# Kernel tuning notes

Measured on AMD Instinct MI355X. Metric: run time of the kernel, lower is better.

Reference implementation:

```python
import jax, jax.numpy as jnp
import numpy as np

B, SEQ, D = 4, 1024, 1024
H = 16
HD = D // H            # 64, matches cos/sin last dim
S_COLS, TOPK = 8, 2
INTER = 768            # find_multiple(round(1.0 * D * 2 / 3), 256)
EPS = 1e-5


def setup_inputs() -> dict:
    key = jax.random.key(0)
    ks = jax.random.split(key, 6)
    hidden_states = jax.random.normal(ks[0], (B, SEQ, D), jnp.float32)
    # RoPE tables (standard rotary, theta=10000)
    inv_freq = 1.0 / (10000.0 ** (jnp.arange(0, HD, 2, dtype=jnp.float32) / HD))
    freqs = jnp.outer(jnp.arange(SEQ, dtype=jnp.float32), inv_freq)
    emb = jnp.concatenate([freqs, freqs], axis=-1)  # [SEQ, HD]
    cos, sin = jnp.cos(emb), jnp.sin(emb)
    Wr = jax.random.normal(ks[1], (S_COLS, D), jnp.float32) * 0.02
    temperature = jnp.ones((1,), jnp.float32)
    # Stacked per-column TransformerBlock params (bias-free linears)
    Wqkv = jax.random.normal(ks[2], (S_COLS, D, 3 * D), jnp.float32) * 0.02
    Wo = jax.random.normal(ks[3], (S_COLS, D, D), jnp.float32) * 0.02
    Wgu = jax.random.normal(ks[4], (S_COLS, D, 2 * INTER), jnp.float32) * 0.02
    Wd = jax.random.normal(ks[5], (S_COLS, INTER, D), jnp.float32) * 0.02
    return dict(hidden_states=hidden_states, cos=cos, sin=sin, Wr=Wr,
                temperature=temperature, Wqkv=Wqkv, Wo=Wo, Wgu=Wgu, Wd=Wd)


def _rms_norm(x):
    return x * jax.lax.rsqrt(jnp.mean(x * x, axis=-1, keepdims=True) + EPS)


def _rotate_half(x):
    x1, x2 = jnp.split(x, 2, axis=-1)
    return jnp.concatenate([-x2, x1], axis=-1)


def _columns_forward(x, Wqkv, Wo, Wgu, Wd, cos, sin):
    # x: [n, seq, D] dispatched sequences; params gathered per dispatch entry [n, ...]
    n, seq, d = x.shape
    qkv = jnp.einsum('nsd,nde->nse', x, Wqkv)
    q, k, v = jnp.split(qkv, 3, axis=-1)
    q = q.reshape(n, seq, H, HD)
    k = k.reshape(n, seq, H, HD)
    v = v.reshape(n, seq, H, HD)
    c = cos[None, :, None, :]
    s = sin[None, :, None, :]
    q = q * c + _rotate_half(q) * s
    k = k * c + _rotate_half(k) * s
    scores = jnp.einsum('nqhd,nkhd->nhqk', q, k) / jnp.sqrt(jnp.asarray(HD, x.dtype))
    attn = jax.nn.softmax(scores, axis=-1)  # non-causal (HRM-style block)
    ctx = jnp.einsum('nhqk,nkhd->nqhd', attn, v).reshape(n, seq, d)
    attn_out = jnp.einsum('nsd,nde->nse', ctx, Wo)
    x = _rms_norm(x + attn_out)                      # post-norm residual
    gu = jnp.einsum('nsd,nde->nse', x, Wgu)
    gate, up = jnp.split(gu, 2, axis=-1)
    mlp_out = jnp.einsum('nsi,nid->nsd', jax.nn.silu(gate) * up, Wd)
    return _rms_norm(x + mlp_out)


def reference(hidden_states, cos, sin, Wr, temperature, Wqkv, Wo, Wgu, Wd):
    Bn = hidden_states.shape[0]
    temp = jnp.clip(temperature, 0.1, 10.0)
    routing_logits = (hidden_states.mean(axis=1) @ Wr.T) / temp   # [B, S]
    topk_vals, topk_idx = jax.lax.top_k(routing_logits, TOPK)
    weights = jax.nn.softmax(topk_vals, axis=-1)                  # [B, k]
    flat_idx = topk_idx.reshape(-1)                               # [B*k] expert ids
    flat_w = weights.reshape(-1)
    sample_idx = jnp.repeat(jnp.arange(Bn), TOPK)                 # [B*k]
    # Sparse dispatch: exactly B*k block forwards via per-entry param gather
    x_disp = hidden_states[sample_idx]
    col_out = _columns_forward(x_disp, Wqkv[flat_idx], Wo[flat_idx],
                               Wgu[flat_idx], Wd[flat_idx], cos, sin)
    result = jnp.zeros_like(hidden_states).at[sample_idx].add(
        flat_w[:, None, None] * col_out)
    return result, routing_logits
```

## Files before the change

kernel.cpp:

```cpp
#include <hip/hip_runtime.h>
#include <hip/hip_bf16.h>
#include <math.h>

#define B_     4
#define SEQ_   1024
#define D_     1024
#define H_     16
#define NE_    8
#define INTER_ 768
#define EPS_   1e-5f

typedef unsigned short u16;
typedef __attribute__((ext_vector_type(8))) short s8v;
typedef __attribute__((ext_vector_type(4))) short s4v;
typedef __attribute__((ext_vector_type(4))) float f4v;
typedef __attribute__((ext_vector_type(4))) unsigned short u16x4;
typedef __attribute__((ext_vector_type(8))) unsigned short u16x8;

__device__ __forceinline__ u16 f2bf(float x) {
    union { float f; unsigned u; } c; c.f = x;
    unsigned r = (c.u + 0x7FFFu + ((c.u >> 16) & 1u)) >> 16;
    return (u16)r;
}
__device__ __forceinline__ float bf2f(u16 h) {
    union { unsigned u; float f; } c; c.u = ((unsigned)h) << 16;
    return c.f;
}
__device__ __forceinline__ unsigned pk2(float a, float b) {
    union { float f; unsigned u; } x, y; x.f = a; y.f = b;
    return ((x.u + 0x8000u) >> 16) | ((y.u + 0x8000u) & 0xffff0000u);
}

#define GLDS16(gp, lp) \
    __builtin_amdgcn_global_load_lds((const __attribute__((address_space(1))) unsigned int*)(gp), \
                                     (__attribute__((address_space(3))) unsigned int*)(lp), 16, 0, 0)

__global__ void route1(const float* __restrict__ hidden, float* __restrict__ part) {
    int b = blockIdx.x, ch = blockIdx.y, t = threadIdx.x;
    const float* xb = hidden + (size_t)b * SEQ_ * D_ + (size_t)ch * 32 * D_;
    float4 acc = make_float4(0.f, 0.f, 0.f, 0.f);
    for (int r = 0; r < 32; ++r) {
        float4 v = *(const float4*)&xb[(size_t)r * D_ + t * 4];
        acc.x += v.x; acc.y += v.y; acc.z += v.z; acc.w += v.w;
    }
    *(float4*)&part[((size_t)(b * 32 + ch)) * D_ + t * 4] = acc;
}

__global__ void route2(const float* __restrict__ part, const float* __restrict__ Wr,
                       const float* __restrict__ temp, float* __restrict__ out_logits,
                       int* __restrict__ flat_idx, float* __restrict__ flat_w) {
    __shared__ float col[1024];
    __shared__ float sm[8];
    int b = blockIdx.x, t = threadIdx.x;
    float4 s = make_float4(0.f, 0.f, 0.f, 0.f);
    for (int ch = 0; ch < 32; ++ch) {
        float4 v = *(const float4*)&part[((size_t)(b * 32 + ch)) * D_ + t * 4];
        s.x += v.x; s.y += v.y; s.z += v.z; s.w += v.w;
    }
    col[t * 4 + 0] = s.x * (1.f / 1024.f);
    col[t * 4 + 1] = s.y * (1.f / 1024.f);
    col[t * 4 + 2] = s.z * (1.f / 1024.f);
    col[t * 4 + 3] = s.w * (1.f / 1024.f);
    __syncthreads();
    int j = t >> 5, d0 = t & 31;
    float p = 0.f;
    for (int d = d0; d < 1024; d += 32) p += col[d] * Wr[j * 1024 + d];
    for (int off = 16; off >= 1; off >>= 1) p += __shfl_down(p, off, 32);
    if (d0 == 0) sm[j] = p;
    __syncthreads();
    if (t == 0) {
        float tc = temp[0];
        tc = fminf(fmaxf(tc, 0.1f), 10.0f);
        float lg[8];
        for (int jj = 0; jj < 8; ++jj) {
            lg[jj] = sm[jj] / tc;
            out_logits[b * 8 + jj] = lg[jj];
        }
        int i0 = 0; float v0 = lg[0];
        for (int jj = 1; jj < 8; ++jj) if (lg[jj] > v0) { v0 = lg[jj]; i0 = jj; }
        int i1 = -1; float v1 = -1e30f;
        for (int jj = 0; jj < 8; ++jj) if (jj != i0 && lg[jj] > v1) { v1 = lg[jj]; i1 = jj; }
        float e1 = expf(v1 - v0);
        flat_idx[2 * b]     = i0;
        flat_idx[2 * b + 1] = i1;
        flat_w[2 * b]       = 1.0f / (1.0f + e1);
        flat_w[2 * b + 1]   = e1 / (1.0f + e1);
    }
}

__global__ __launch_bounds__(256) void wtrans(const float* __restrict__ W, u16* __restrict__ Wt,
                                              int K, int N) {
    __shared__ float tile[64][65];
    int e = blockIdx.z;
    int k0 = blockIdx.y * 64, n0 = blockIdx.x * 64;
    const float* Wp = W + (size_t)e * K * N;
    u16* Wtp = Wt + (size_t)e * K * N;
    int t = threadIdx.x;
    int kk = t >> 4, ns = t & 15;
#pragma unroll
    for (int p = 0; p < 4; ++p) {
        float4 v = *(const float4*)&Wp[(size_t)(k0 + kk + p * 16) * N + n0 + ns * 4];
        tile[kk + p * 16][ns * 4 + 0] = v.x;
        tile[kk + p * 16][ns * 4 + 1] = v.y;
        tile[kk + p * 16][ns * 4 + 2] = v.z;
        tile[kk + p * 16][ns * 4 + 3] = v.w;
    }
    __syncthreads();
    int nn = t >> 3, ks = t & 7;
#pragma unroll
    for (int p = 0; p < 2; ++p) {
        u16x8 o;
#pragma unroll
        for (int jj = 0; jj < 8; ++jj) o[jj] = f2bf(tile[ks * 8 + jj][nn + p * 32]);
        *(u16x8*)&Wtp[(size_t)(n0 + nn + p * 32) * K + k0 + ks * 8] = o;
    }
}

__global__ void cast_hidden(const float* __restrict__ x, u16* __restrict__ xb) {
    size_t i = (size_t)blockIdx.x * 256 + threadIdx.x;
    float4 v = *(const float4*)&x[i * 4];
    u16x4 o = {f2bf(v.x), f2bf(v.y), f2bf(v.z), f2bf(v.w)};
    *(u16x4*)&xb[i * 4] = o;
}

template<int OUTBF>
__global__ __launch_bounds__(256) void gemm_bf16(const u16* __restrict__ Abase,
                                                 const u16* __restrict__ Wtbase,
                                                 void* __restrict__ Cb,
                                                 const int* __restrict__ flat_idx,
                                                 int M, int N, int K, int aDiv) {
    __shared__ __align__(16) u16 As[128 * 32];
    __shared__ __align__(16) u16 Bs[128 * 32];
    int e = blockIdx.z;
    const u16* A  = Abase + (size_t)(e / aDiv) * M * K;
    const u16* Wt = Wtbase + (size_t)flat_idx[e] * N * K;
    int m0 = blockIdx.y * 128, n0 = blockIdx.x * 128;
    int t = threadIdx.x, lane = t & 63, w = t >> 6;
    int g = lane >> 4, c = lane & 15;
    int wm = (w >> 1) * 64, wn = (w & 1) * 64;

    f4v acc[4][4];
#pragma unroll
    for (int i = 0; i < 4; ++i)
#pragma unroll
        for (int jj = 0; jj < 4; ++jj) acc[i][jj] = (f4v){0.f, 0.f, 0.f, 0.f};

    for (int k0 = 0; k0 < K; k0 += 32) {
#pragma unroll
        for (int it = 0; it < 2; ++it) {
            int p = it * 256 + w * 64 + lane;
            int row = p >> 2, seg = p & 3;
            GLDS16(A  + (size_t)(m0 + row) * K + k0 + seg * 8, As + (size_t)(it * 256 + w * 64) * 8);
            GLDS16(Wt + (size_t)(n0 + row) * K + k0 + seg * 8, Bs + (size_t)(it * 256 + w * 64) * 8);
        }
        __syncthreads();
        s8v af[4], bfr[4];
#pragma unroll
        for (int ti = 0; ti < 4; ++ti) af[ti]  = *(const s8v*)&As[(wm + ti * 16 + c) * 32 + g * 8];
#pragma unroll
        for (int tj = 0; tj < 4; ++tj) bfr[tj] = *(const s8v*)&Bs[(wn + tj * 16 + c) * 32 + g * 8];
#pragma unroll
        for (int ti = 0; ti < 4; ++ti)
#pragma unroll
            for (int tj = 0; tj < 4; ++tj)
                acc[ti][tj] = __builtin_amdgcn_mfma_f32_16x16x32_bf16(af[ti], bfr[tj], acc[ti][tj], 0, 0, 0);
        __syncthreads();
    }
    if (OUTBF) {
        u16* C = (u16*)Cb + (size_t)e * M * N;
#pragma unroll
        for (int ti = 0; ti < 4; ++ti)
#pragma unroll
            for (int tj = 0; tj < 4; ++tj)
#pragma unroll
                for (int i = 0; i < 4; ++i)
                    C[(size_t)(m0 + wm + ti * 16 + g * 4 + i) * N + n0 + wn + tj * 16 + c] = f2bf(acc[ti][tj][i]);
    } else {
        float* C = (float*)Cb + (size_t)e * M * N;
#pragma unroll
        for (int ti = 0; ti < 4; ++ti)
#pragma unroll
            for (int tj = 0; tj < 4; ++tj)
#pragma unroll
                for (int i = 0; i < 4; ++i)
                    C[(size_t)(m0 + wm + ti * 16 + g * 4 + i) * N + n0 + wn + tj * 16 + c] = acc[ti][tj][i];
    }
}

__global__ void rope_cast(const u16* __restrict__ qkvb, const float* __restrict__ cosb,
                          const float* __restrict__ sinb, u16* __restrict__ Qb, u16* __restrict__ Kb) {
    int idx = blockIdx.x * 256 + threadIdx.x;
    int seg = idx & 3, h = (idx >> 2) & 15, s = (idx >> 6) & 1023, e = idx >> 16;
    int d0 = seg * 8;
    size_t base = ((size_t)(e * 1024) + s) * 3072 + h * 64;
    size_t ob   = ((size_t)(e * 1024) + s) * 1024 + h * 64;
    u16x8 qlo = *(const u16x8*)&qkvb[base + d0];
    u16x8 qhi = *(const u16x8*)&qkvb[base + d0 + 32];
    u16x8 klo = *(const u16x8*)&qkvb[base + 1024 + d0];
    u16x8 khi = *(const u16x8*)&qkvb[base + 1024 + d0 + 32];
    float c1[8], c2[8], s1[8], s2[8];
    *(float4*)&c1[0] = *(const float4*)&cosb[s * 64 + d0];
    *(float4*)&c1[4] = *(const float4*)&cosb[s * 64 + d0 + 4];
    *(float4*)&c2[0] = *(const float4*)&cosb[s * 64 + d0 + 32];
    *(float4*)&c2[4] = *(const float4*)&cosb[s * 64 + d0 + 36];
    *(float4*)&s1[0] = *(const float4*)&sinb[s * 64 + d0];
    *(float4*)&s1[4] = *(const float4*)&sinb[s * 64 + d0 + 4];
    *(float4*)&s2[0] = *(const float4*)&sinb[s * 64 + d0 + 32];
    *(float4*)&s2[4] = *(const float4*)&sinb[s * 64 + d0 + 36];
    const float SQ = 0.125f * 1.44269504f;
    u16x8 qol, qoh, kol, koh;
#pragma unroll
    for (int jj = 0; jj < 8; ++jj) {
        float q1 = bf2f(qlo[jj]), q2 = bf2f(qhi[jj]);
        qol[jj] = f2bf((q1 * c1[jj] - q2 * s1[jj]) * SQ);
        qoh[jj] = f2bf((q2 * c2[jj] + q1 * s2[jj]) * SQ);
        float k1 = bf2f(klo[jj]), k2 = bf2f(khi[jj]);
        kol[jj] = f2bf(k1 * c1[jj] - k2 * s1[jj]);
        koh[jj] = f2bf(k2 * c2[jj] + k1 * s2[jj]);
    }
    *(u16x8*)&Qb[ob + d0]      = qol;
    *(u16x8*)&Qb[ob + d0 + 32] = qoh;
    *(u16x8*)&Kb[ob + d0]      = kol;
    *(u16x8*)&Kb[ob + d0 + 32] = koh;
}

__global__ __launch_bounds__(256) void vtrans(const u16* __restrict__ qkvb, u16* __restrict__ Vtg) {
    __shared__ __align__(16) u16 tile[64 * 72];
    int s0 = blockIdx.x * 64;
    int eh = blockIdx.y;
    int e = eh >> 4, h = eh & 15;
    int t = threadIdx.x;
#pragma unroll
    for (int it = 0; it < 2; ++it) {
        int p = it * 256 + t;
        int sr = p >> 3, ds = p & 7;
        u16x8 v = *(const u16x8*)&qkvb[((size_t)(e * 1024) + s0 + sr) * 3072 + 2048 + h * 64 + ds * 8];
        *(u16x8*)&tile[sr * 72 + ds * 8] = v;
    }
    __syncthreads();
#pragma unroll
    for (int it = 0; it < 2; ++it) {
        int p = it * 256 + t;
        int d = p >> 3, ks = p & 7;
        u16x8 o;
#pragma unroll
        for (int jj = 0; jj < 8; ++jj) o[jj] = tile[(ks * 8 + jj) * 72 + d];
        *(u16x8*)&Vtg[((size_t)((e * 16 + h) * 64) + d) * 1024 + s0 + ks * 8] = o;
    }
}

__global__ __launch_bounds__(256) void attn_mfma(const u16* __restrict__ Qb, const u16* __restrict__ Kb,
                                                 const u16* __restrict__ Vtg, u16* __restrict__ ctx) {
    __shared__ __align__(16) u16 Ks[64 * 64];
    __shared__ __align__(16) u16 Vt[64 * 64];
    int e = blockIdx.x, h = blockIdx.y, qt = blockIdx.z;
    int t = threadIdx.x, lane = t & 63, w = t >> 6;
    int g = lane >> 4, c = lane & 15;
    int q0 = qt * 64 + w * 16;

    s8v qf[2];
#pragma unroll
    for (int ks = 0; ks < 2; ++ks)
        qf[ks] = *(const s8v*)&Qb[((size_t)(e * 1024) + q0 + c) * 1024 + h * 64 + ks * 32 + g * 8];

    f4v O[4];
#pragma unroll
    for (int tj = 0; tj < 4; ++tj) O[tj] = (f4v){0.f, 0.f, 0.f, 0.f};
    f4v liacc = (f4v){0.f, 0.f, 0.f, 0.f};
    const s4v vone = {(short)0x3F80, (short)0x3F80, (short)0x3F80, (short)0x3F80};

    for (int kt = 0; kt < 16; ++kt) {
#pragma unroll
        for (int it = 0; it < 2; ++it) {
            int p = it * 256 + w * 64 + lane;
            int row = p >> 3, ss = p & 7;
            GLDS16(Kb + ((size_t)(e * 1024 + kt * 64 + row)) * 1024 + h * 64 + (ss ^ (row & 7)) * 8,
                   Ks + (size_t)(it * 256 + w * 64) * 8);
            GLDS16(Vtg + ((size_t)((e * 16 + h) * 64 + row)) * 1024 + kt * 64 + (ss ^ (row & 7)) * 8,
                   Vt + (size_t)(it * 256 + w * 64) * 8);
        }
        __syncthreads();

        f4v st[4];
#pragma unroll
        for (int tj = 0; tj < 4; ++tj) st[tj] = (f4v){0.f, 0.f, 0.f, 0.f};
#pragma unroll
        for (int ks = 0; ks < 2; ++ks)
#pragma unroll
            for (int tj = 0; tj < 4; ++tj) {
                int kvl = tj * 16 + c;
                s8v kf = *(const s8v*)&Ks[kvl * 64 + (((ks * 4 + g) ^ (kvl & 7)) * 8)];
                st[tj] = __builtin_amdgcn_mfma_f32_16x16x32_bf16(kf, qf[ks], st[tj], 0, 0, 0);
            }

        s4v pf[4];
#pragma unroll
        for (int tj = 0; tj < 4; ++tj) {
            float p0 = __builtin_amdgcn_exp2f(st[tj][0]);
            float p1 = __builtin_amdgcn_exp2f(st[tj][1]);
            float p2 = __builtin_amdgcn_exp2f(st[tj][2]);
            float p3 = __builtin_amdgcn_exp2f(st[tj][3]);
            union { unsigned u[2]; s4v v; } pu;
            pu.u[0] = pk2(p0, p1);
            pu.u[1] = pk2(p2, p3);
            pf[tj] = pu.v;
        }

#pragma unroll
        for (int tjC = 0; tjC < 4; ++tjC) {
            liacc = __builtin_amdgcn_mfma_f32_16x16x16bf16_1k(pf[tjC], vone, liacc, 0, 0, 0);
#pragma unroll
            for (int tjd = 0; tjd < 4; ++tjd) {
                int d = tjd * 16 + c;
                int sd = tjC * 2 + (g >> 1);
                s4v vf = *(const s4v*)&Vt[d * 64 + ((sd ^ (d & 7)) * 8) + (g & 1) * 4];
                O[tjd] = __builtin_amdgcn_mfma_f32_16x16x16bf16_1k(pf[tjC], vf, O[tjd], 0, 0, 0);
            }
        }
        __syncthreads();
    }
#pragma unroll
    for (int i = 0; i < 4; ++i) {
        float linv = 1.0f / liacc[i];
        size_t rbase = ((size_t)(e * 1024) + q0 + g * 4 + i) * 1024 + h * 64;
#pragma unroll
        for (int tjd = 0; tjd < 4; ++tjd)
            ctx[rbase + tjd * 16 + c] = f2bf(O[tjd][i] * linv);
    }
}

__global__ void add_rmsnorm(const float* __restrict__ hidden, const float* __restrict__ ao,
                            u16* __restrict__ xnb) {
    int row = blockIdx.x;
    int e = row >> 10;
    int b = e >> 1;
    int s = row & 1023;
    const float* xr = hidden + (((size_t)b * SEQ_ + s) << 10);
    const float* ar = ao + ((size_t)row << 10);
    u16* o = xnb + ((size_t)row << 10);
    int t = threadIdx.x;
    float v[4];
    float ss = 0.f;
#pragma unroll
    for (int i = 0; i < 4; ++i) {
        v[i] = xr[t + i * 256] + ar[t + i * 256];
        ss += v[i] * v[i];
    }
    for (int off = 32; off >= 1; off >>= 1) ss += __shfl_down(ss, off, 64);
    __shared__ float wred[4];
    if ((t & 63) == 0) wred[t >> 6] = ss;
    __syncthreads();
    float tot = wred[0] + wred[1] + wred[2] + wred[3];
    float scale = rsqrtf(tot * (1.0f / 1024.0f) + EPS_);
#pragma unroll
    for (int i = 0; i < 4; ++i) o[t + i * 256] = f2bf(v[i] * scale);
}

__global__ void silu_mul(const u16* __restrict__ gub, u16* __restrict__ act) {
    int idx = blockIdx.x * 256 + threadIdx.x;
    int col8 = idx % 96;
    int row  = idx / 96;
    u16x8 gv = *(const u16x8*)&gub[(size_t)row * 1536 + col8 * 8];
    u16x8 uv = *(const u16x8*)&gub[(size_t)row * 1536 + 768 + col8 * 8];
    u16x8 o;
#pragma unroll
    for (int jj = 0; jj < 8; ++jj) {
        float gt = bf2f(gv[jj]), u = bf2f(uv[jj]);
        o[jj] = f2bf(gt / (1.f + __expf(-gt)) * u);
    }
    *(u16x8*)&act[(size_t)row * 768 + col8 * 8] = o;
}

__global__ void final_kernel(const u16* __restrict__ xnb, const float* __restrict__ mlp,
                             const float* __restrict__ flat_w, float* __restrict__ out) {
    int row = blockIdx.x;
    int b = row >> 10;
    int s = row & 1023;
    int t = threadIdx.x;
    __shared__ float wred[4];
    float res[4] = {0.f, 0.f, 0.f, 0.f};
    for (int j = 0; j < 2; ++j) {
        int e = 2 * b + j;
        size_t off = (((size_t)e * SEQ_ + s) << 10);
        const u16* xr = xnb + off;
        const float* mr = mlp + off;
        float v[4];
        float ss = 0.f;
#pragma unroll
        for (int i = 0; i < 4; ++i) {
            v[i] = bf2f(xr[t + i * 256]) + mr[t + i * 256];
            ss += v[i] * v[i];
        }
        for (int off2 = 32; off2 >= 1; off2 >>= 1) ss += __shfl_down(ss, off2, 64);
        if ((t & 63) == 0) wred[t >> 6] = ss;
        __syncthreads();
        float tot = wred[0] + wred[1] + wred[2] + wred[3];
        float scale = rsqrtf(tot * (1.0f / 1024.0f) + EPS_);
        float wgt = flat_w[e];
#pragma unroll
        for (int i = 0; i < 4; ++i) res[i] += wgt * v[i] * scale;
        __syncthreads();
    }
    float* o = out + ((size_t)row << 10);
#pragma unroll
    for (int i = 0; i < 4; ++i) o[t + i * 256] = res[i];
}

extern "C" void kernel_launch(void* const* d_in, const int* in_sizes, int n_in,
                              void* d_out, int out_size, void* d_ws, size_t ws_size,
                              hipStream_t stream) {
    const float* hidden = (const float*)d_in[0];
    const float* cosb   = (const float*)d_in[1];
    const float* sinb   = (const float*)d_in[2];
    const float* Wr     = (const float*)d_in[3];
    const float* temp   = (const float*)d_in[4];
    const float* Wqkv   = (const float*)d_in[5];
    const float* Wo     = (const float*)d_in[6];
    const float* Wgu    = (const float*)d_in[7];
    const float* Wd     = (const float*)d_in[8];
    float* out = (float*)d_out;
    float* out_logits = out + (size_t)B_ * SEQ_ * D_;

    char* base = (char*)d_ws;
    int*   flat_idx = (int*)base;
    float* flat_w   = (float*)(base + 128);
    float* routeP   = (float*)(base + 4096);
    size_t off = (size_t)1 << 20;
    u16* WqkvT = (u16*)(base + off); off += (size_t)8 * 3072 * 1024 * 2;
    u16* WoT   = (u16*)(base + off); off += (size_t)8 * 1024 * 1024 * 2;
    u16* WguT  = (u16*)(base + off); off += (size_t)8 * 1536 * 1024 * 2;
    u16* WdT   = (u16*)(base + off); off += (size_t)8 * 1024 * 768 * 2;
    u16* hb    = (u16*)(base + off); off += (size_t)4 * 1024 * 1024 * 2;
    u16* qkvb  = (u16*)(base + off); off += (size_t)8 * 1024 * 3072 * 2;
    u16* Qb    = (u16*)(base + off); off += (size_t)8 * 1024 * 1024 * 2;
    u16* Kb    = (u16*)(base + off); off += (size_t)8 * 1024 * 1024 * 2;
    u16* Vtg   = (u16*)(base + off); off += (size_t)8 * 1024 * 1024 * 2;
    u16* ctxb  = (u16*)(base + off); off += (size_t)8 * 1024 * 1024 * 2;
    float* R1  = (float*)(base + off); off += (size_t)8 * 1024 * 1024 * 4;
    u16* xnb   = (u16*)(base + off); off += (size_t)8 * 1024 * 1024 * 2;
    u16* gub   = qkvb;
    u16* actb  = qkvb + (size_t)8 * 1024 * 1536;

    route1<<<dim3(4, 32), 256, 0, stream>>>(hidden, routeP);
    route2<<<4, 256, 0, stream>>>(routeP, Wr, temp, out_logits, flat_idx, flat_w);
    cast_hidden<<<4096, 256, 0, stream>>>(hidden, hb);
    wtrans<<<dim3(48, 16, 8), 256, 0, stream>>>(Wqkv, WqkvT, 1024, 3072);
    wtrans<<<dim3(16, 16, 8), 256, 0, stream>>>(Wo, WoT, 1024, 1024);
    wtrans<<<dim3(24, 16, 8), 256, 0, stream>>>(Wgu, WguT, 1024, 1536);
    wtrans<<<dim3(16, 12, 8), 256, 0, stream>>>(Wd, WdT, 768, 1024);

    gemm_bf16<1><<<dim3(24, 8, 8), 256, 0, stream>>>(hb, WqkvT, qkvb, flat_idx, 1024, 3072, 1024, 2);
    rope_cast<<<2048, 256, 0, stream>>>(qkvb, cosb, sinb, Qb, Kb);
    vtrans<<<dim3(16, 128), 256, 0, stream>>>(qkvb, Vtg);
    attn_mfma<<<dim3(8, 16, 16), 256, 0, stream>>>(Qb, Kb, Vtg, ctxb);
    gemm_bf16<0><<<dim3(8, 8, 8), 256, 0, stream>>>(ctxb, WoT, R1, flat_idx, 1024, 1024, 1024, 1);
    add_rmsnorm<<<NE_ * SEQ_, 256, 0, stream>>>(hidden, R1, xnb);
    gemm_bf16<1><<<dim3(12, 8, 8), 256, 0, stream>>>(xnb, WguT, gub, flat_idx, 1024, 1536, 1024, 1);
    silu_mul<<<3072, 256, 0, stream>>>(gub, actb);
    gemm_bf16<0><<<dim3(8, 8, 8), 256, 0, stream>>>(actb, WdT, R1, flat_idx, 1024, 1024, 768, 1);
    final_kernel<<<B_ * SEQ_, 256, 0, stream>>>(xnb, R1, flat_w, out);
}
```

Measured before the change: 591.1 us.

## Fuse RoPE into QKV GEMM epilogue and swizzle GEMM LDS layout

Folds the RoPE rotation and Q scaling into the QKV GEMM epilogue, so Q and K are written directly and V goes to a separate buffer that reuses the R1 workspace. This removes the rope_cast kernel and one round trip of the QKV intermediate through memory. It also adds an XOR swizzle to the shared-memory tile layout in all GEMMs to cut LDS bank conflicts on fragment reads. In exchange, the epilogue stores are scalar 16-bit writes with per-element cos and sin loads, which may coalesce poorly.

Result: faster. 573.2 us (-3.0%).

```diff
diff --git a/kernel.cpp b/kernel.cpp
--- a/kernel.cpp
+++ b/kernel.cpp
@@ -123,6 +123,33 @@
     *(u16x4*)&xb[i * 4] = o;
 }
 
+#define GEMM_CORE(A, Wt, K)                                                                 \
+    f4v acc[4][4];                                                                          \
+    _Pragma("unroll") for (int i = 0; i < 4; ++i)                                           \
+        _Pragma("unroll") for (int jj = 0; jj < 4; ++jj) acc[i][jj] = (f4v){0.f,0.f,0.f,0.f}; \
+    for (int k0 = 0; k0 < K; k0 += 32) {                                                    \
+        _Pragma("unroll") for (int it = 0; it < 2; ++it) {                                  \
+            int p = it * 256 + w * 64 + lane;                                               \
+            int row = p >> 2, seg = (p & 3) ^ ((row >> 1) & 3);                             \
+            GLDS16(A  + (size_t)(m0 + row) * K + k0 + seg * 8, As + (size_t)(it*256 + w*64) * 8); \
+            GLDS16(Wt + (size_t)(n0 + row) * K + k0 + seg * 8, Bs + (size_t)(it*256 + w*64) * 8); \
+        }                                                                                   \
+        __syncthreads();                                                                    \
+        s8v af[4], bfr[4];                                                                  \
+        _Pragma("unroll") for (int ti = 0; ti < 4; ++ti) {                                  \
+            int r = wm + ti * 16 + c;                                                       \
+            af[ti]  = *(const s8v*)&As[r * 32 + (g ^ ((r >> 1) & 3)) * 8];                   \
+        }                                                                                   \
+        _Pragma("unroll") for (int tj = 0; tj < 4; ++tj) {                                  \
+            int r = wn + tj * 16 + c;                                                       \
+            bfr[tj] = *(const s8v*)&Bs[r * 32 + (g ^ ((r >> 1) & 3)) * 8];                   \
+        }                                                                                   \
+        _Pragma("unroll") for (int ti = 0; ti < 4; ++ti)                                    \
+            _Pragma("unroll") for (int tj = 0; tj < 4; ++tj)                                \
+                acc[ti][tj] = __builtin_amdgcn_mfma_f32_16x16x32_bf16(af[ti], bfr[tj], acc[ti][tj], 0, 0, 0); \
+        __syncthreads();                                                                    \
+    }
+
 template<int OUTBF>
 __global__ __launch_bounds__(256) void gemm_bf16(const u16* __restrict__ Abase,
                                                  const u16* __restrict__ Wtbase,
@@ -139,33 +166,8 @@
     int g = lane >> 4, c = lane & 15;
     int wm = (w >> 1) * 64, wn = (w & 1) * 64;
 
-    f4v acc[4][4];
-#pragma unroll
-    for (int i = 0; i < 4; ++i)
-#pragma unroll
-        for (int jj = 0; jj < 4; ++jj) acc[i][jj] = (f4v){0.f, 0.f, 0.f, 0.f};
-
-    for (int k0 = 0; k0 < K; k0 += 32) {
-#pragma unroll
-        for (int it = 0; it < 2; ++it) {
-            int p = it * 256 + w * 64 + lane;
-            int row = p >> 2, seg = p & 3;
-            GLDS16(A  + (size_t)(m0 + row) * K + k0 + seg * 8, As + (size_t)(it * 256 + w * 64) * 8);
-            GLDS16(Wt + (size_t)(n0 + row) * K + k0 + seg * 8, Bs + (size_t)(it * 256 + w * 64) * 8);
-        }
-        __syncthreads();
-        s8v af[4], bfr[4];
-#pragma unroll
-        for (int ti = 0; ti < 4; ++ti) af[ti]  = *(const s8v*)&As[(wm + ti * 16 + c) * 32 + g * 8];
-#pragma unroll
-        for (int tj = 0; tj < 4; ++tj) bfr[tj] = *(const s8v*)&Bs[(wn + tj * 16 + c) * 32 + g * 8];
-#pragma unroll
-        for (int ti = 0; ti < 4; ++ti)
-#pragma unroll
-            for (int tj = 0; tj < 4; ++tj)
-                acc[ti][tj] = __builtin_amdgcn_mfma_f32_16x16x32_bf16(af[ti], bfr[tj], acc[ti][tj], 0, 0, 0);
-        __syncthreads();
-    }
+    GEMM_CORE(A, Wt, K)
+
     if (OUTBF) {
         u16* C = (u16*)Cb + (size_t)e * M * N;
 #pragma unroll
@@ -187,44 +189,62 @@
     }
 }
 
-__global__ void rope_cast(const u16* __restrict__ qkvb, const float* __restrict__ cosb,
-                          const float* __restrict__ sinb, u16* __restrict__ Qb, u16* __restrict__ Kb) {
-    int idx = blockIdx.x * 256 + threadIdx.x;
-    int seg = idx & 3, h = (idx >> 2) & 15, s = (idx >> 6) & 1023, e = idx >> 16;
-    int d0 = seg * 8;
-    size_t base = ((size_t)(e * 1024) + s) * 3072 + h * 64;
-    size_t ob   = ((size_t)(e * 1024) + s) * 1024 + h * 64;
-    u16x8 qlo = *(const u16x8*)&qkvb[base + d0];
-    u16x8 qhi = *(const u16x8*)&qkvb[base + d0 + 32];
-    u16x8 klo = *(const u16x8*)&qkvb[base + 1024 + d0];
-    u16x8 khi = *(const u16x8*)&qkvb[base + 1024 + d0 + 32];
-    float c1[8], c2[8], s1[8], s2[8];
-    *(float4*)&c1[0] = *(const float4*)&cosb[s * 64 + d0];
-    *(float4*)&c1[4] = *(const float4*)&cosb[s * 64 + d0 + 4];
-    *(float4*)&c2[0] = *(const float4*)&cosb[s * 64 + d0 + 32];
-    *(float4*)&c2[4] = *(const float4*)&cosb[s * 64 + d0 + 36];
-    *(float4*)&s1[0] = *(const float4*)&sinb[s * 64 + d0];
-    *(float4*)&s1[4] = *(const float4*)&sinb[s * 64 + d0 + 4];
-    *(float4*)&s2[0] = *(const float4*)&sinb[s * 64 + d0 + 32];
-    *(float4*)&s2[4] = *(const float4*)&sinb[s * 64 + d0 + 36];
-    const float SQ = 0.125f * 1.44269504f;
-    u16x8 qol, qoh, kol, koh;
-#pragma unroll
-    for (int jj = 0; jj < 8; ++jj) {
-        float q1 = bf2f(qlo[jj]), q2 = bf2f(qhi[jj]);
-        qol[jj] = f2bf((q1 * c1[jj] - q2 * s1[jj]) * SQ);
-        qoh[jj] = f2bf((q2 * c2[jj] + q1 * s2[jj]) * SQ);
-        float k1 = bf2f(klo[jj]), k2 = bf2f(khi[jj]);
-        kol[jj] = f2bf(k1 * c1[jj] - k2 * s1[jj]);
-        koh[jj] = f2bf(k2 * c2[jj] + k1 * s2[jj]);
-    }
-    *(u16x8*)&Qb[ob + d0]      = qol;
-    *(u16x8*)&Qb[ob + d0 + 32] = qoh;
-    *(u16x8*)&Kb[ob + d0]      = kol;
-    *(u16x8*)&Kb[ob + d0 + 32] = koh;
-}
-
-__global__ __launch_bounds__(256) void vtrans(const u16* __restrict__ qkvb, u16* __restrict__ Vtg) {
+__global__ __launch_bounds__(256) void gemm_qkv(const u16* __restrict__ Abase,
+                                                const u16* __restrict__ Wtbase,
+                                                const int* __restrict__ flat_idx,
+                                                const float* __restrict__ cosb,
+                                                const float* __restrict__ sinb,
+                                                u16* __restrict__ Qb, u16* __restrict__ Kb,
+                                                u16* __restrict__ Vb) {
+    __shared__ __align__(16) u16 As[128 * 32];
+    __shared__ __align__(16) u16 Bs[128 * 32];
+    const int K = 1024, N = 3072;
+    int e = blockIdx.z;
+    const u16* A  = Abase + (size_t)(e >> 1) * 1024 * K;
+    const u16* Wt = Wtbase + (size_t)flat_idx[e] * N * K;
+    int m0 = blockIdx.y * 128, n0 = blockIdx.x * 128;
+    int t = threadIdx.x, lane = t & 63, w = t >> 6;
+    int g = lane >> 4, c = lane & 15;
+    int wm = (w >> 1) * 64, wn = (w & 1) * 64;
+
+    GEMM_CORE(A, Wt, K)
+
+    int col0 = n0 + wn;
+    int sb = m0 + wm + g * 4;
+    if (col0 < 2048) {
+        bool isq = col0 < 1024;
+        u16* dst = isq ? Qb : Kb;
+        int h = (col0 & 1023) >> 6;
+        const float scl = isq ? 0.125f * 1.44269504f : 1.0f;
+#pragma unroll
+        for (int ti = 0; ti < 4; ++ti)
+#pragma unroll
+            for (int i = 0; i < 4; ++i) {
+                int s = sb + ti * 16 + i;
+                size_t ob = ((size_t)(e * 1024) + s) * 1024 + h * 64;
+#pragma unroll
+                for (int tj = 0; tj < 2; ++tj) {
+                    int d = tj * 16 + c;
+                    float x1 = acc[ti][tj][i], x2 = acc[ti][tj + 2][i];
+                    float c1 = cosb[s * 64 + d],      s1 = sinb[s * 64 + d];
+                    float c2 = cosb[s * 64 + d + 32], s2 = sinb[s * 64 + d + 32];
+                    dst[ob + d]      = f2bf((x1 * c1 - x2 * s1) * scl);
+                    dst[ob + d + 32] = f2bf((x2 * c2 + x1 * s2) * scl);
+                }
+            }
+    } else {
+        int vcol = col0 - 2048;
+#pragma unroll
+        for (int ti = 0; ti < 4; ++ti)
+#pragma unroll
+            for (int tj = 0; tj < 4; ++tj)
+#pragma unroll
+                for (int i = 0; i < 4; ++i)
+                    Vb[((size_t)(e * 1024) + sb + ti * 16 + i) * 1024 + vcol + tj * 16 + c] = f2bf(acc[ti][tj][i]);
+    }
+}
+
+__global__ __launch_bounds__(256) void vtrans(const u16* __restrict__ Vb, u16* __restrict__ Vtg) {
     __shared__ __align__(16) u16 tile[64 * 72];
     int s0 = blockIdx.x * 64;
     int eh = blockIdx.y;
@@ -234,7 +254,7 @@
     for (int it = 0; it < 2; ++it) {
         int p = it * 256 + t;
         int sr = p >> 3, ds = p & 7;
-        u16x8 v = *(const u16x8*)&qkvb[((size_t)(e * 1024) + s0 + sr) * 3072 + 2048 + h * 64 + ds * 8];
+        u16x8 v = *(const u16x8*)&Vb[((size_t)(e * 1024) + s0 + sr) * 1024 + h * 64 + ds * 8];
         *(u16x8*)&tile[sr * 72 + ds * 8] = v;
     }
     __syncthreads();
@@ -431,15 +451,16 @@
     u16* WguT  = (u16*)(base + off); off += (size_t)8 * 1536 * 1024 * 2;
     u16* WdT   = (u16*)(base + off); off += (size_t)8 * 1024 * 768 * 2;
     u16* hb    = (u16*)(base + off); off += (size_t)4 * 1024 * 1024 * 2;
-    u16* qkvb  = (u16*)(base + off); off += (size_t)8 * 1024 * 3072 * 2;
+    u16* scr   = (u16*)(base + off); off += (size_t)8 * 1024 * 3072 * 2;
     u16* Qb    = (u16*)(base + off); off += (size_t)8 * 1024 * 1024 * 2;
     u16* Kb    = (u16*)(base + off); off += (size_t)8 * 1024 * 1024 * 2;
     u16* Vtg   = (u16*)(base + off); off += (size_t)8 * 1024 * 1024 * 2;
     u16* ctxb  = (u16*)(base + off); off += (size_t)8 * 1024 * 1024 * 2;
     float* R1  = (float*)(base + off); off += (size_t)8 * 1024 * 1024 * 4;
     u16* xnb   = (u16*)(base + off); off += (size_t)8 * 1024 * 1024 * 2;
-    u16* gub   = qkvb;
-    u16* actb  = qkvb + (size_t)8 * 1024 * 1536;
+    u16* gub   = scr;
+    u16* actb  = scr + (size_t)8 * 1024 * 1536;
+    u16* Vb    = (u16*)R1;
 
     route1<<<dim3(4, 32), 256, 0, stream>>>(hidden, routeP);
     route2<<<4, 256, 0, stream>>>(routeP, Wr, temp, out_logits, flat_idx, flat_w);
@@ -449,9 +470,8 @@
     wtrans<<<dim3(24, 16, 8), 256, 0, stream>>>(Wgu, WguT, 1024, 1536);
     wtrans<<<dim3(16, 12, 8), 256, 0, stream>>>(Wd, WdT, 768, 1024);
 
-    gemm_bf16<1><<<dim3(24, 8, 8), 256, 0, stream>>>(hb, WqkvT, qkvb, flat_idx, 1024, 3072, 1024, 2);
-    rope_cast<<<2048, 256, 0, stream>>>(qkvb, cosb, sinb, Qb, Kb);
-    vtrans<<<dim3(16, 128), 256, 0, stream>>>(qkvb, Vtg);
+    gemm_qkv<<<dim3(24, 8, 8), 256, 0, stream>>>(hb, WqkvT, flat_idx, cosb, sinb, Qb, Kb, Vb);
+    vtrans<<<dim3(16, 128), 256, 0, stream>>>(Vb, Vtg);
     attn_mfma<<<dim3(8, 16, 16), 256, 0, stream>>>(Qb, Kb, Vtg, ctxb);
     gemm_bf16<0><<<dim3(8, 8, 8), 256, 0, stream>>>(ctxb, WoT, R1, flat_idx, 1024, 1024, 1024, 1);
     add_rmsnorm<<<NE_ * SEQ_, 256, 0, stream>>>(hidden, R1, xnb);
```
